# Optimization experiments

Measured on AMD Instinct MI355X. Metric: run time of the kernel, lower is better.

Reference implementation:

```python
import jax, jax.numpy as jnp
import numpy as np

D_MODEL = 1024
D_FF = 2 * D_MODEL
N_EXPERTS = 8
TOP_K = 2
SCAT_SCALE = 0.1


def setup_inputs() -> dict:
    key = jax.random.key(0)
    ks = jax.random.split(key, 8)
    s_in = 1.0 / np.sqrt(D_MODEL)
    s_ff = 1.0 / np.sqrt(D_FF)
    return {
        "x": jax.random.normal(ks[0], (4, 2048, D_MODEL), dtype=jnp.float32),
        "Wg": jax.random.uniform(ks[1], (D_MODEL, N_EXPERTS), minval=-s_in, maxval=s_in),
        "bg": jax.random.uniform(ks[2], (N_EXPERTS,), minval=-s_in, maxval=s_in),
        "W1": jax.random.uniform(ks[3], (N_EXPERTS, D_MODEL, D_FF), minval=-s_in, maxval=s_in),
        "b1": jax.random.uniform(ks[4], (N_EXPERTS, D_FF), minval=-s_in, maxval=s_in),
        "W2": jax.random.uniform(ks[5], (N_EXPERTS, D_FF, D_MODEL), minval=-s_ff, maxval=s_ff),
        "b2": jax.random.uniform(ks[6], (N_EXPERTS, D_MODEL), minval=-s_ff, maxval=s_ff),
    }


def reference(x, Wg, bg, W1, b1, W2, b2):
    B, N, D = x.shape
    T = B * N
    xf = x.reshape(T, D)

    # gating logits + norm-based modulation (scattering_scale branch)
    logits = xf @ Wg + bg  # [T, E]
    tnorm = jnp.linalg.norm(xf, axis=-1, keepdims=True)  # [T, 1]
    norm_scaled = (tnorm - tnorm.mean()) / (jnp.std(tnorm, ddof=1) + 1e-6)
    logits = logits + SCAT_SCALE * norm_scaled

    # top-k routing
    topv, topi = jax.lax.top_k(logits, TOP_K)  # [T, K]
    gates_k = jax.nn.softmax(topv, axis=-1)  # [T, K]
    routing_entropy = -(gates_k * jnp.log(jnp.clip(gates_k, 1e-8, None))).sum(-1).mean()

    # dense per-token expert-weight matrix (zeros for non-selected experts)
    E = W1.shape[0]
    gates = jnp.zeros((T, E), dtype=gates_k.dtype).at[
        jnp.arange(T)[:, None], topi
    ].add(gates_k)  # [T, E]

    # all-expert MLP (dense equivalent of sparse dispatch; weight 0 -> no contribution)
    h = jax.nn.relu(jnp.einsum("td,edf->etf", xf, W1) + b1[:, None, :])  # [E, T, F]
    y = jnp.einsum("etf,efd->etd", h, W2) + b2[:, None, :]  # [E, T, D]
    out = jnp.einsum("etd,te->td", y, gates).reshape(B, N, D)
    return out, routing_entropy
```

## Files before the change

### kernel.cpp

```cpp
#include <hip/hip_runtime.h>
#include <hip/hip_bf16.h>

#define T_TOK 8192
#define DMODEL 1024
#define DFF 2048
#define NEXP 8

typedef __attribute__((ext_vector_type(8))) short short8v;
typedef __attribute__((ext_vector_type(4))) float floatx4;
typedef __attribute__((ext_vector_type(4))) ushort ushort4v;

__device__ __forceinline__ ushort f2bf(float f) {
  union { float f; unsigned u; } v; v.f = f;
  unsigned u = v.u;
  unsigned r = (u + 0x7FFFu + ((u >> 16) & 1u)) >> 16;
  return (ushort)r;
}
__device__ __forceinline__ float bf2f(ushort b) {
  union { unsigned u; float f; } v; v.u = ((unsigned)b) << 16;
  return v.f;
}
__device__ __forceinline__ void gload16(const void* g, void* l) {
  __builtin_amdgcn_global_load_lds(
      (const __attribute__((address_space(1))) unsigned int*)g,
      (__attribute__((address_space(3))) unsigned int*)l, 16, 0, 0);
}
__device__ __forceinline__ short8v dsr128(unsigned off) {
  short8v r;
  asm volatile("ds_read_b128 %0, %1" : "=v"(r) : "v"(off));
  return r;
}
#define VMW(n) asm volatile("s_waitcnt vmcnt(" #n ")" ::: "memory")
#define LG0()  asm volatile("s_waitcnt lgkmcnt(0)" ::: "memory")
#define BAR()  asm volatile("s_barrier" ::: "memory")
#define SB0()  __builtin_amdgcn_sched_barrier(0)

__global__ void init_kernel(int* __restrict__ meta, float* __restrict__ entWs) {
  if (threadIdx.x < 64) meta[threadIdx.x] = 0;
  if (threadIdx.x == 0) *entWs = 0.f;
}

__global__ __launch_bounds__(256) void gating_kernel(
    const float* __restrict__ x, const float* __restrict__ Wg,
    const float* __restrict__ bg, int* __restrict__ meta,
    int* __restrict__ te, float* __restrict__ tg, float* __restrict__ entWs,
    ushort* __restrict__ xb) {
  __shared__ float wgT[8448];
  __shared__ float sbg[NEXP];
  __shared__ int cnt_s[NEXP];
  __shared__ float ent_s;
  int tid = threadIdx.x;
#pragma unroll
  for (int k = 0; k < 8; ++k) {
    int g4 = tid + 256 * k;
    float4 v = ((const float4*)Wg)[g4];
    int q = g4 * 4;
    int f = q >> 5;
    wgT[q + f]     = v.x;
    wgT[q + 1 + f] = v.y;
    wgT[q + 2 + f] = v.z;
    wgT[q + 3 + f] = v.w;
  }
  if (tid < NEXP) { sbg[tid] = bg[tid]; cnt_s[tid] = 0; }
  if (tid == 0) ent_s = 0.f;
  __syncthreads();

  int wid = tid >> 6, lane = tid & 63;
#pragma unroll 1
  for (int it = 0; it < 4; ++it) {
    int t = blockIdx.x * 16 + wid * 4 + it;
    const float* xr = x + (long)t * DMODEL;
    ushort* xbr = xb + (long)t * DMODEL;
    float acc[NEXP];
#pragma unroll
    for (int e = 0; e < NEXP; ++e) acc[e] = 0.f;
#pragma unroll
    for (int i = 0; i < 4; ++i) {
      int dbase = i * 256 + lane * 4;
      int pad = i * 64 + lane;
      float4 xv = *(const float4*)(xr + dbase);
      ushort4v s;
      s[0] = f2bf(xv.x); s[1] = f2bf(xv.y); s[2] = f2bf(xv.z); s[3] = f2bf(xv.w);
      *(ushort4v*)(xbr + dbase) = s;
      float xj[4] = {xv.x, xv.y, xv.z, xv.w};
#pragma unroll
      for (int j = 0; j < 4; ++j) {
        int base = 8 * (dbase + j) + pad;
#pragma unroll
        for (int e = 0; e < NEXP; ++e) acc[e] += xj[j] * wgT[base + e];
      }
    }
#pragma unroll
    for (int off = 32; off; off >>= 1)
#pragma unroll
      for (int e = 0; e < NEXP; ++e) acc[e] += __shfl_xor(acc[e], off, 64);
    if (lane == 0) {
      float lg[NEXP];
#pragma unroll
      for (int e = 0; e < NEXP; ++e) lg[e] = acc[e] + sbg[e];
      int e1 = 0; float v1 = lg[0];
#pragma unroll
      for (int e = 1; e < NEXP; ++e) if (lg[e] > v1) { v1 = lg[e]; e1 = e; }
      int e2 = -1; float v2 = -1e30f;
#pragma unroll
      for (int e = 0; e < NEXP; ++e) if (e != e1 && lg[e] > v2) { v2 = lg[e]; e2 = e; }
      float p2 = expf(v2 - v1);
      float s = 1.f + p2;
      float g1 = 1.f / s, g2 = p2 / s;
      float ent = -(g1 * logf(fmaxf(g1, 1e-8f)) + g2 * logf(fmaxf(g2, 1e-8f)));
      atomicAdd(&cnt_s[e1], 1);
      atomicAdd(&cnt_s[e2], 1);
      atomicAdd(&ent_s, ent);
      te[2 * t] = e1; te[2 * t + 1] = e2;
      tg[2 * t] = g1; tg[2 * t + 1] = g2;
    }
  }
  __syncthreads();
  if (tid < NEXP && cnt_s[tid]) atomicAdd(&meta[tid], cnt_s[tid]);
  if (tid == 0) atomicAdd(entWs, ent_s * (1.f / T_TOK));
}

__global__ void prefix_kernel(int* __restrict__ meta) {
  if (threadIdx.x == 0) {
    int s = 0;
    for (int e = 0; e < NEXP; ++e) { meta[16 + e] = s; s += meta[e]; meta[32 + e] = 0; }
  }
}

__global__ void scatter_kernel(const int* __restrict__ te, const float* __restrict__ tg,
                               int* __restrict__ meta, int* __restrict__ tok,
                               float* __restrict__ gate, int* __restrict__ slotOf) {
  int t = blockIdx.x * blockDim.x + threadIdx.x;
  if (t >= T_TOK) return;
  for (int k = 0; k < 2; ++k) {
    int e = te[2 * t + k];
    int pos = atomicAdd(&meta[32 + e], 1);
    int slot = meta[16 + e] + pos;
    tok[slot] = t;
    gate[slot] = tg[2 * t + k];
    slotOf[2 * t + k] = slot;
  }
}

__global__ __launch_bounds__(256) void tcvt2_kernel(
    const float* __restrict__ W1, const float* __restrict__ W2,
    ushort* __restrict__ w1t, ushort* __restrict__ w2t) {
  int id = blockIdx.x;
  const float* src; ushort* dst; int R, C, r0, c0, e;
  if (id < 4096) {
    src = W1; dst = w1t; R = DMODEL; C = DFF;
    c0 = (id & 31) * 64; r0 = ((id >> 5) & 15) * 64; e = id >> 9;
  } else {
    int j = id - 4096;
    src = W2; dst = w2t; R = DFF; C = DMODEL;
    c0 = (j & 15) * 64; r0 = ((j >> 4) & 31) * 64; e = j >> 9;
  }
  __shared__ ushort tile[64][72];
  int tid = threadIdx.x;
  long eoff = (long)e * R * C;
  int lr = tid >> 4, lc = (tid & 15) * 4;
#pragma unroll
  for (int p = 0; p < 4; ++p) {
    int r = lr + p * 16;
    float4 v = *(const float4*)&src[eoff + (long)(r0 + r) * C + (c0 + lc)];
    tile[r][lc + 0] = f2bf(v.x); tile[r][lc + 1] = f2bf(v.y);
    tile[r][lc + 2] = f2bf(v.z); tile[r][lc + 3] = f2bf(v.w);
  }
  __syncthreads();
  int sr = tid >> 3, sc = (tid & 7) * 8;
#pragma unroll
  for (int p = 0; p < 2; ++p) {
    int c = sr + p * 32;
    short8v v;
#pragma unroll
    for (int j = 0; j < 8; ++j) v[j] = (short)tile[sc + j][c];
    *(short8v*)&dst[eoff + (long)(c0 + c) * R + (r0 + sc)] = v;
  }
}

__device__ __forceinline__ void gemm_pipe(
    int NT, const char* aP0, const char* aP1, const char* bP0, const char* bP1,
    char* lds, int tid, floatx4 (&acc)[4][4]) {
  const unsigned ldsU = (unsigned)(unsigned long)lds;
  int lane = tid & 63, wid = tid >> 6;
  int lr = lane & 15, lg = lane >> 4;
  int wm = (wid >> 1) * 64, wn = (wid & 1) * 64;
  unsigned offA[4], offB[4];
#pragma unroll
  for (int mi = 0; mi < 4; ++mi) {
    int row = wm + mi * 16 + lr;
    offA[mi] = row * 64 + ((lg * 16) ^ (((row >> 1) & 3) << 4));
  }
#pragma unroll
  for (int ni = 0; ni < 4; ++ni) {
    int row = wn + ni * 16 + lr;
    offB[ni] = row * 64 + ((lg * 16) ^ (((row >> 1) & 3) << 4));
  }

  auto STG = [&](int b, int t) {
    int koff = t * 64;
    char* da = lds + b * 8192;
    gload16(aP0 + koff, da + tid * 16);
    gload16(aP1 + koff, da + 4096 + tid * 16);
    char* db = lds + 24576 + b * 8192;
    gload16(bP0 + koff, db + tid * 16);
    gload16(bP1 + koff, db + 4096 + tid * 16);
  };
  auto RD = [&](int b, short8v (&af)[4], short8v (&bf)[4]) {
#pragma unroll
    for (int ni = 0; ni < 4; ++ni) bf[ni] = dsr128(ldsU + 24576u + (unsigned)(b * 8192) + offB[ni]);
#pragma unroll
    for (int mi = 0; mi < 4; ++mi) af[mi] = dsr128(ldsU + (unsigned)(b * 8192) + offA[mi]);
  };
  auto MM = [&](short8v (&af)[4], short8v (&bf)[4]) {
#pragma unroll
    for (int mi = 0; mi < 4; ++mi)
#pragma unroll
      for (int ni = 0; ni < 4; ++ni)
        acc[mi][ni] =
            __builtin_amdgcn_mfma_f32_16x16x32_bf16(af[mi], bf[ni], acc[mi][ni], 0, 0, 0);
  };

  STG(0, 0); STG(1, 1);

  short8v af[4], bf[4];
  int b = 0;
#pragma unroll 1
  for (int t = 0; t < NT; ++t) {
    if (t == NT - 1) { VMW(0); } else { VMW(4); }
    BAR();
    RD(b, af, bf);
    if (t + 2 < NT) STG((b + 2 >= 3) ? b - 1 : b + 2, t + 2);
    LG0(); SB0();
    __builtin_amdgcn_s_setprio(1); MM(af, bf); __builtin_amdgcn_s_setprio(0);
    SB0();
    b = (b == 2) ? 0 : b + 1;
  }
}

__global__ __launch_bounds__(256, 3) void gemm1_kernel(
    const ushort* __restrict__ xb, const ushort* __restrict__ w1t,
    const float* __restrict__ b1, const int* __restrict__ meta,
    const int* __restrict__ tok, ushort* __restrict__ h) {
  const int NWG = 64 * 16 * NEXP;
  int flat = blockIdx.x;
  int wgid = (flat % 8) * (NWG / 8) + flat / 8;
  int m0 = (wgid & 63) * 128;
  int rest = wgid >> 6;
  int n0 = (rest & 15) * 128;
  int e = rest >> 4;
  int cnt = meta[e];
  if (m0 >= cnt) return;
  int bas = meta[16 + e];
  __shared__ char lds[49152];
  int tid = threadIdx.x;

  const char* w1e = (const char*)(w1t + (long)e * DFF * DMODEL);
  int rA = tid >> 2;
  int ch = tid & 3;
  auto sc = [&](int row) { return (unsigned)((ch * 16) ^ (((row >> 1) & 3) << 4)); };
  int ma0 = m0 + rA;        if (ma0 >= cnt) ma0 = cnt - 1;
  int ma1 = m0 + rA + 64;   if (ma1 >= cnt) ma1 = cnt - 1;
  const char* aP0 = (const char*)xb + (long)tok[bas + ma0] * (DMODEL * 2) + sc(rA);
  const char* aP1 = (const char*)xb + (long)tok[bas + ma1] * (DMODEL * 2) + sc(rA + 64);
  const char* bP0 = w1e + (long)(n0 + rA) * (DMODEL * 2) + sc(rA);
  const char* bP1 = w1e + (long)(n0 + rA + 64) * (DMODEL * 2) + sc(rA + 64);

  floatx4 acc[4][4];
#pragma unroll
  for (int i = 0; i < 4; ++i)
#pragma unroll
    for (int j = 0; j < 4; ++j) acc[i][j] = (floatx4){0.f, 0.f, 0.f, 0.f};

  gemm_pipe(DMODEL / 32, aP0, aP1, bP0, bP1, lds, tid, acc);

  int lane = tid & 63, wid = tid >> 6;
  int lr = lane & 15, lg = lane >> 4;
  int wm = (wid >> 1) * 64, wn = (wid & 1) * 64;
  const float* b1e = b1 + e * DFF;
#pragma unroll
  for (int mi = 0; mi < 4; ++mi) {
#pragma unroll
    for (int r = 0; r < 4; ++r) {
      int m = m0 + wm + mi * 16 + lg * 4 + r;
      if (m >= cnt) continue;
      long hrow = (long)(bas + m) * DFF;
#pragma unroll
      for (int ni = 0; ni < 4; ++ni) {
        int f = n0 + wn + ni * 16 + lr;
        float v = acc[mi][ni][r] + b1e[f];
        h[hrow + f] = f2bf(fmaxf(v, 0.f));
      }
    }
  }
}

__global__ __launch_bounds__(256, 3) void gemm2_kernel(
    const ushort* __restrict__ h, const ushort* __restrict__ w2t,
    const float* __restrict__ b2, const int* __restrict__ meta,
    const float* __restrict__ gate, ushort* __restrict__ y) {
  const int NWG = 64 * 8 * NEXP;
  int flat = blockIdx.x;
  int wgid = (flat % 8) * (NWG / 8) + flat / 8;
  int m0 = (wgid & 63) * 128;
  int rest = wgid >> 6;
  int n0 = (rest & 7) * 128;
  int e = rest >> 3;
  int cnt = meta[e];
  if (m0 >= cnt) return;
  int bas = meta[16 + e];
  __shared__ char lds[49152];
  int tid = threadIdx.x;

  const char* w2e = (const char*)(w2t + (long)e * DMODEL * DFF);
  int rA = tid >> 2;
  int ch = tid & 3;
  auto sc = [&](int row) { return (unsigned)((ch * 16) ^ (((row >> 1) & 3) << 4)); };
  int ma0 = m0 + rA;        if (ma0 >= cnt) ma0 = cnt - 1;
  int ma1 = m0 + rA + 64;   if (ma1 >= cnt) ma1 = cnt - 1;
  const char* aP0 = (const char*)h + (long)(bas + ma0) * (DFF * 2) + sc(rA);
  const char* aP1 = (const char*)h + (long)(bas + ma1) * (DFF * 2) + sc(rA + 64);
  const char* bP0 = w2e + (long)(n0 + rA) * (DFF * 2) + sc(rA);
  const char* bP1 = w2e + (long)(n0 + rA + 64) * (DFF * 2) + sc(rA + 64);

  floatx4 acc[4][4];
#pragma unroll
  for (int i = 0; i < 4; ++i)
#pragma unroll
    for (int j = 0; j < 4; ++j) acc[i][j] = (floatx4){0.f, 0.f, 0.f, 0.f};

  gemm_pipe(DFF / 32, aP0, aP1, bP0, bP1, lds, tid, acc);

  int lane = tid & 63, wid = tid >> 6;
  int lr = lane & 15, lg = lane >> 4;
  int wm = (wid >> 1) * 64, wn = (wid & 1) * 64;
  const float* b2e = b2 + e * DMODEL;
#pragma unroll
  for (int mi = 0; mi < 4; ++mi) {
#pragma unroll
    for (int r = 0; r < 4; ++r) {
      int m = m0 + wm + mi * 16 + lg * 4 + r;
      if (m >= cnt) continue;
      int slot = bas + m;
      float g = gate[slot];
      ushort* yr = y + (long)slot * DMODEL;
#pragma unroll
      for (int ni = 0; ni < 4; ++ni) {
        int n = n0 + wn + ni * 16 + lr;
        float v = g * (acc[mi][ni][r] + b2e[n]);
        yr[n] = f2bf(v);
      }
    }
  }
}

__global__ __launch_bounds__(256) void combine_kernel(
    const ushort* __restrict__ y, const int* __restrict__ slotOf,
    const float* __restrict__ entWs, float* __restrict__ out) {
  int t = blockIdx.x;
  int s1 = slotOf[2 * t], s2 = slotOf[2 * t + 1];
  int d = threadIdx.x * 4;
  ushort4v a = *(const ushort4v*)&y[(long)s1 * DMODEL + d];
  ushort4v b = *(const ushort4v*)&y[(long)s2 * DMODEL + d];
  float4 r;
  r.x = bf2f(a[0]) + bf2f(b[0]);
  r.y = bf2f(a[1]) + bf2f(b[1]);
  r.z = bf2f(a[2]) + bf2f(b[2]);
  r.w = bf2f(a[3]) + bf2f(b[3]);
  *(float4*)&out[(long)t * DMODEL + d] = r;
  if (t == 0 && threadIdx.x == 0) out[(long)T_TOK * DMODEL] = *entWs;
}

extern "C" void kernel_launch(void* const* d_in, const int* in_sizes, int n_in,
                              void* d_out, int out_size, void* d_ws, size_t ws_size,
                              hipStream_t stream) {
  const float* x  = (const float*)d_in[0];
  const float* Wg = (const float*)d_in[1];
  const float* bg = (const float*)d_in[2];
  const float* W1 = (const float*)d_in[3];
  const float* b1 = (const float*)d_in[4];
  const float* W2 = (const float*)d_in[5];
  const float* b2 = (const float*)d_in[6];
  float* out = (float*)d_out;

  char* ws = (char*)d_ws;
  int*    meta   = (int*)(ws + 0);
  float*  entWs  = (float*)(ws + 256);
  int*    te     = (int*)(ws + 1024);
  float*  tg     = (float*)(ws + 66560);
  int*    tokA   = (int*)(ws + 132096);
  float*  gate   = (float*)(ws + 197632);
  int*    slotOf = (int*)(ws + 263168);
  ushort* xb     = (ushort*)(ws + 328704);
  ushort* w1t    = (ushort*)(ws + 17105920);
  ushort* w2t    = (ushort*)(ws + 50660352);
  ushort* h      = (ushort*)(ws + 84214784);
  ushort* y      = w1t;

  init_kernel<<<1, 64, 0, stream>>>(meta, entWs);
  gating_kernel<<<T_TOK / 16, 256, 0, stream>>>(x, Wg, bg, meta, te, tg, entWs, xb);
  prefix_kernel<<<1, 1, 0, stream>>>(meta);
  scatter_kernel<<<T_TOK / 256, 256, 0, stream>>>(te, tg, meta, tokA, gate, slotOf);
  tcvt2_kernel<<<8192, 256, 0, stream>>>(W1, W2, w1t, w2t);
  gemm1_kernel<<<64 * 16 * NEXP, 256, 0, stream>>>(xb, w1t, b1, meta, tokA, h);
  gemm2_kernel<<<64 * 8 * NEXP, 256, 0, stream>>>(h, w2t, b2, meta, gate, y);
  combine_kernel<<<T_TOK, 256, 0, stream>>>(y, slotOf, entWs, out);
}
```

Measured before the change: 339.5 us.

## Switch expert GEMMs to single-wave 64x128 workgroups without barriers

Both expert GEMM kernels now use one 64-lane wavefront per workgroup computing a 64x128 tile, instead of four waves sharing a 128x128 tile. This removes the s_barrier from the K loop and changes the LDS ring from three stages to two, each holding one combined A+B tile, with each lane issuing 12 direct-to-LDS loads per step. The grid doubles along M and the accumulators grow to 4x8 MFMA tiles per wave. The cost is less operand reuse per workgroup, since each A tile is shared by half as many columns, more global and LDS traffic per FLOP, and a higher register count per wave.

```diff
diff --git a/kernel.cpp b/kernel.cpp
--- a/kernel.cpp
+++ b/kernel.cpp
@@ -32,7 +32,6 @@
 }
 #define VMW(n) asm volatile("s_waitcnt vmcnt(" #n ")" ::: "memory")
 #define LG0()  asm volatile("s_waitcnt lgkmcnt(0)" ::: "memory")
-#define BAR()  asm volatile("s_barrier" ::: "memory")
 #define SB0()  __builtin_amdgcn_sched_barrier(0)
 
 __global__ void init_kernel(int* __restrict__ meta, float* __restrict__ entWs) {
@@ -179,115 +178,110 @@
 }
 
 __device__ __forceinline__ void gemm_pipe(
-    int NT, const char* aP0, const char* aP1, const char* bP0, const char* bP1,
-    char* lds, int tid, floatx4 (&acc)[4][4]) {
+    int NT, const char* const* aS, const char* const* bS,
+    char* lds, int lane, floatx4 (&acc)[4][8]) {
   const unsigned ldsU = (unsigned)(unsigned long)lds;
-  int lane = tid & 63, wid = tid >> 6;
   int lr = lane & 15, lg = lane >> 4;
-  int wm = (wid >> 1) * 64, wn = (wid & 1) * 64;
-  unsigned offA[4], offB[4];
+  unsigned offA[4], offB[8];
 #pragma unroll
   for (int mi = 0; mi < 4; ++mi) {
-    int row = wm + mi * 16 + lr;
+    int row = mi * 16 + lr;
     offA[mi] = row * 64 + ((lg * 16) ^ (((row >> 1) & 3) << 4));
   }
 #pragma unroll
-  for (int ni = 0; ni < 4; ++ni) {
-    int row = wn + ni * 16 + lr;
-    offB[ni] = row * 64 + ((lg * 16) ^ (((row >> 1) & 3) << 4));
+  for (int ni = 0; ni < 8; ++ni) {
+    int row = ni * 16 + lr;
+    offB[ni] = 4096 + row * 64 + ((lg * 16) ^ (((row >> 1) & 3) << 4));
   }
 
   auto STG = [&](int b, int t) {
     int koff = t * 64;
-    char* da = lds + b * 8192;
-    gload16(aP0 + koff, da + tid * 16);
-    gload16(aP1 + koff, da + 4096 + tid * 16);
-    char* db = lds + 24576 + b * 8192;
-    gload16(bP0 + koff, db + tid * 16);
-    gload16(bP1 + koff, db + 4096 + tid * 16);
+    char* d = lds + b * 12288;
+#pragma unroll
+    for (int i = 0; i < 4; ++i) gload16(aS[i] + koff, d + i * 1024 + lane * 16);
+#pragma unroll
+    for (int i = 0; i < 8; ++i) gload16(bS[i] + koff, d + 4096 + i * 1024 + lane * 16);
   };
-  auto RD = [&](int b, short8v (&af)[4], short8v (&bf)[4]) {
-#pragma unroll
-    for (int ni = 0; ni < 4; ++ni) bf[ni] = dsr128(ldsU + 24576u + (unsigned)(b * 8192) + offB[ni]);
-#pragma unroll
-    for (int mi = 0; mi < 4; ++mi) af[mi] = dsr128(ldsU + (unsigned)(b * 8192) + offA[mi]);
-  };
-  auto MM = [&](short8v (&af)[4], short8v (&bf)[4]) {
+
+  STG(0, 0); STG(1, 1);
+
+  short8v af[4], bf[8];
+#pragma unroll 1
+  for (int t = 0; t < NT; ++t) {
+    if (t >= NT - 1) { VMW(0); } else { VMW(12); }
+    unsigned base = ldsU + (unsigned)((t & 1) * 12288);
+#pragma unroll
+    for (int ni = 0; ni < 8; ++ni) bf[ni] = dsr128(base + offB[ni]);
+#pragma unroll
+    for (int mi = 0; mi < 4; ++mi) af[mi] = dsr128(base + offA[mi]);
+    LG0(); SB0();
+    if (t + 2 < NT) STG(t & 1, t + 2);
+    __builtin_amdgcn_s_setprio(1);
 #pragma unroll
     for (int mi = 0; mi < 4; ++mi)
 #pragma unroll
-      for (int ni = 0; ni < 4; ++ni)
+      for (int ni = 0; ni < 8; ++ni)
         acc[mi][ni] =
             __builtin_amdgcn_mfma_f32_16x16x32_bf16(af[mi], bf[ni], acc[mi][ni], 0, 0, 0);
-  };
-
-  STG(0, 0); STG(1, 1);
-
-  short8v af[4], bf[4];
-  int b = 0;
-#pragma unroll 1
-  for (int t = 0; t < NT; ++t) {
-    if (t == NT - 1) { VMW(0); } else { VMW(4); }
-    BAR();
-    RD(b, af, bf);
-    if (t + 2 < NT) STG((b + 2 >= 3) ? b - 1 : b + 2, t + 2);
-    LG0(); SB0();
-    __builtin_amdgcn_s_setprio(1); MM(af, bf); __builtin_amdgcn_s_setprio(0);
+    __builtin_amdgcn_s_setprio(0);
     SB0();
-    b = (b == 2) ? 0 : b + 1;
-  }
-}
-
-__global__ __launch_bounds__(256, 3) void gemm1_kernel(
+  }
+}
+
+__global__ __launch_bounds__(64) void gemm1_kernel(
     const ushort* __restrict__ xb, const ushort* __restrict__ w1t,
     const float* __restrict__ b1, const int* __restrict__ meta,
     const int* __restrict__ tok, ushort* __restrict__ h) {
-  const int NWG = 64 * 16 * NEXP;
+  const int NWG = 128 * 16 * NEXP;
   int flat = blockIdx.x;
   int wgid = (flat % 8) * (NWG / 8) + flat / 8;
-  int m0 = (wgid & 63) * 128;
-  int rest = wgid >> 6;
+  int m0 = (wgid & 127) * 64;
+  int rest = wgid >> 7;
   int n0 = (rest & 15) * 128;
   int e = rest >> 4;
   int cnt = meta[e];
   if (m0 >= cnt) return;
   int bas = meta[16 + e];
-  __shared__ char lds[49152];
-  int tid = threadIdx.x;
+  __shared__ char lds[24576];
+  int lane = threadIdx.x;
 
   const char* w1e = (const char*)(w1t + (long)e * DFF * DMODEL);
-  int rA = tid >> 2;
-  int ch = tid & 3;
+  int rr = lane >> 2, ch = lane & 3;
   auto sc = [&](int row) { return (unsigned)((ch * 16) ^ (((row >> 1) & 3) << 4)); };
-  int ma0 = m0 + rA;        if (ma0 >= cnt) ma0 = cnt - 1;
-  int ma1 = m0 + rA + 64;   if (ma1 >= cnt) ma1 = cnt - 1;
-  const char* aP0 = (const char*)xb + (long)tok[bas + ma0] * (DMODEL * 2) + sc(rA);
-  const char* aP1 = (const char*)xb + (long)tok[bas + ma1] * (DMODEL * 2) + sc(rA + 64);
-  const char* bP0 = w1e + (long)(n0 + rA) * (DMODEL * 2) + sc(rA);
-  const char* bP1 = w1e + (long)(n0 + rA + 64) * (DMODEL * 2) + sc(rA + 64);
-
-  floatx4 acc[4][4];
+  const char* aS[4];
+  const char* bS[8];
+#pragma unroll
+  for (int i = 0; i < 4; ++i) {
+    int r = i * 16 + rr;
+    int m = m0 + r; if (m >= cnt) m = cnt - 1;
+    aS[i] = (const char*)xb + (long)tok[bas + m] * (DMODEL * 2) + sc(r);
+  }
+#pragma unroll
+  for (int i = 0; i < 8; ++i) {
+    int r = i * 16 + rr;
+    bS[i] = w1e + (long)(n0 + r) * (DMODEL * 2) + sc(r);
+  }
+
+  floatx4 acc[4][8];
 #pragma unroll
   for (int i = 0; i < 4; ++i)
 #pragma unroll
-    for (int j = 0; j < 4; ++j) acc[i][j] = (floatx4){0.f, 0.f, 0.f, 0.f};
-
-  gemm_pipe(DMODEL / 32, aP0, aP1, bP0, bP1, lds, tid, acc);
-
-  int lane = tid & 63, wid = tid >> 6;
+    for (int j = 0; j < 8; ++j) acc[i][j] = (floatx4){0.f, 0.f, 0.f, 0.f};
+
+  gemm_pipe(DMODEL / 32, aS, bS, lds, lane, acc);
+
   int lr = lane & 15, lg = lane >> 4;
-  int wm = (wid >> 1) * 64, wn = (wid & 1) * 64;
   const float* b1e = b1 + e * DFF;
 #pragma unroll
   for (int mi = 0; mi < 4; ++mi) {
 #pragma unroll
     for (int r = 0; r < 4; ++r) {
-      int m = m0 + wm + mi * 16 + lg * 4 + r;
+      int m = m0 + mi * 16 + lg * 4 + r;
       if (m >= cnt) continue;
       long hrow = (long)(bas + m) * DFF;
 #pragma unroll
-      for (int ni = 0; ni < 4; ++ni) {
-        int f = n0 + wn + ni * 16 + lr;
+      for (int ni = 0; ni < 8; ++ni) {
+        int f = n0 + ni * 16 + lr;
         float v = acc[mi][ni][r] + b1e[f];
         h[hrow + f] = f2bf(fmaxf(v, 0.f));
       }
@@ -295,58 +289,62 @@
   }
 }
 
-__global__ __launch_bounds__(256, 3) void gemm2_kernel(
+__global__ __launch_bounds__(64) void gemm2_kernel(
     const ushort* __restrict__ h, const ushort* __restrict__ w2t,
     const float* __restrict__ b2, const int* __restrict__ meta,
     const float* __restrict__ gate, ushort* __restrict__ y) {
-  const int NWG = 64 * 8 * NEXP;
+  const int NWG = 128 * 8 * NEXP;
   int flat = blockIdx.x;
   int wgid = (flat % 8) * (NWG / 8) + flat / 8;
-  int m0 = (wgid & 63) * 128;
-  int rest = wgid >> 6;
+  int m0 = (wgid & 127) * 64;
+  int rest = wgid >> 7;
   int n0 = (rest & 7) * 128;
   int e = rest >> 3;
   int cnt = meta[e];
   if (m0 >= cnt) return;
   int bas = meta[16 + e];
-  __shared__ char lds[49152];
-  int tid = threadIdx.x;
+  __shared__ char lds[24576];
+  int lane = threadIdx.x;
 
   const char* w2e = (const char*)(w2t + (long)e * DMODEL * DFF);
-  int rA = tid >> 2;
-  int ch = tid & 3;
+  int rr = lane >> 2, ch = lane & 3;
   auto sc = [&](int row) { return (unsigned)((ch * 16) ^ (((row >> 1) & 3) << 4)); };
-  int ma0 = m0 + rA;        if (ma0 >= cnt) ma0 = cnt - 1;
-  int ma1 = m0 + rA + 64;   if (ma1 >= cnt) ma1 = cnt - 1;
-  const char* aP0 = (const char*)h + (long)(bas + ma0) * (DFF * 2) + sc(rA);
-  const char* aP1 = (const char*)h + (long)(bas + ma1) * (DFF * 2) + sc(rA + 64);
-  const char* bP0 = w2e + (long)(n0 + rA) * (DFF * 2) + sc(rA);
-  const char* bP1 = w2e + (long)(n0 + rA + 64) * (DFF * 2) + sc(rA + 64);
-
-  floatx4 acc[4][4];
+  const char* aS[4];
+  const char* bS[8];
+#pragma unroll
+  for (int i = 0; i < 4; ++i) {
+    int r = i * 16 + rr;
+    int m = m0 + r; if (m >= cnt) m = cnt - 1;
+    aS[i] = (const char*)h + (long)(bas + m) * (DFF * 2) + sc(r);
+  }
+#pragma unroll
+  for (int i = 0; i < 8; ++i) {
+    int r = i * 16 + rr;
+    bS[i] = w2e + (long)(n0 + r) * (DFF * 2) + sc(r);
+  }
+
+  floatx4 acc[4][8];
 #pragma unroll
   for (int i = 0; i < 4; ++i)
 #pragma unroll
-    for (int j = 0; j < 4; ++j) acc[i][j] = (floatx4){0.f, 0.f, 0.f, 0.f};
-
-  gemm_pipe(DFF / 32, aP0, aP1, bP0, bP1, lds, tid, acc);
-
-  int lane = tid & 63, wid = tid >> 6;
+    for (int j = 0; j < 8; ++j) acc[i][j] = (floatx4){0.f, 0.f, 0.f, 0.f};
+
+  gemm_pipe(DFF / 32, aS, bS, lds, lane, acc);
+
   int lr = lane & 15, lg = lane >> 4;
-  int wm = (wid >> 1) * 64, wn = (wid & 1) * 64;
   const float* b2e = b2 + e * DMODEL;
 #pragma unroll
   for (int mi = 0; mi < 4; ++mi) {
 #pragma unroll
     for (int r = 0; r < 4; ++r) {
-      int m = m0 + wm + mi * 16 + lg * 4 + r;
+      int m = m0 + mi * 16 + lg * 4 + r;
       if (m >= cnt) continue;
       int slot = bas + m;
       float g = gate[slot];
       ushort* yr = y + (long)slot * DMODEL;
 #pragma unroll
-      for (int ni = 0; ni < 4; ++ni) {
-        int n = n0 + wn + ni * 16 + lr;
+      for (int ni = 0; ni < 8; ++ni) {
+        int n = n0 + ni * 16 + lr;
         float v = g * (acc[mi][ni][r] + b2e[n]);
         yr[n] = f2bf(v);
       }
@@ -402,7 +400,7 @@
   prefix_kernel<<<1, 1, 0, stream>>>(meta);
   scatter_kernel<<<T_TOK / 256, 256, 0, stream>>>(te, tg, meta, tokA, gate, slotOf);
   tcvt2_kernel<<<8192, 256, 0, stream>>>(W1, W2, w1t, w2t);
-  gemm1_kernel<<<64 * 16 * NEXP, 256, 0, stream>>>(xb, w1t, b1, meta, tokA, h);
-  gemm2_kernel<<<64 * 8 * NEXP, 256, 0, stream>>>(h, w2t, b2, meta, gate, y);
+  gemm1_kernel<<<128 * 16 * NEXP, 64, 0, stream>>>(xb, w1t, b1, meta, tokA, h);
+  gemm2_kernel<<<128 * 8 * NEXP, 64, 0, stream>>>(h, w2t, b2, meta, gate, y);
   combine_kernel<<<T_TOK, 256, 0, stream>>>(y, slotOf, entWs, out);
 }
```

Measured after the change: 413.2 us. 21.7% more time.
